# Optimization experiments

Hardware: AMD Instinct MI355X
Metric: run time of the kernel (lower is better)

The kernel has to match this reference:

```python
import jax, jax.numpy as jnp
import numpy as np

H = 16
D_MODEL = 1024
D_K = D_MODEL // H
B, S = 4, 2048


def setup_inputs() -> dict:
    key = jax.random.key(0)
    ks = jax.random.split(key, 8)
    scale = 1.0 / np.sqrt(D_MODEL)
    return {
        "query": jax.random.normal(ks[0], (B, S, D_MODEL), dtype=jnp.float32),
        "key": jax.random.normal(ks[1], (B, S, D_MODEL), dtype=jnp.float32),
        "value": jax.random.normal(ks[2], (B, S, D_MODEL), dtype=jnp.float32),
        "A": jnp.zeros((1,), dtype=jnp.float32),
        "Wq": jax.random.normal(ks[3], (D_MODEL, D_MODEL), dtype=jnp.float32) * scale,
        "bq": jnp.zeros((D_MODEL,), dtype=jnp.float32),
        "Wk": jax.random.normal(ks[4], (D_MODEL, D_MODEL), dtype=jnp.float32) * scale,
        "bk": jnp.zeros((D_MODEL,), dtype=jnp.float32),
        "Wv": jax.random.normal(ks[5], (D_MODEL, D_MODEL), dtype=jnp.float32) * scale,
        "bv": jnp.zeros((D_MODEL,), dtype=jnp.float32),
        "Wo": jax.random.normal(ks[6], (D_MODEL, D_MODEL), dtype=jnp.float32) * scale,
        "bo": jnp.zeros((D_MODEL,), dtype=jnp.float32),
    }


def reference(query, key, value, A, Wq, bq, Wk, bk, Wv, bv, Wo, bo):
    nb = query.shape[0]

    def proj(x, W, b):
        # torch Linear: x @ W.T + b, then view(B, S, H, D_K) and transpose -> [B, H, S, D_K]
        y = jnp.einsum('bsd,ed->bse', x, W) + b
        return y.reshape(nb, -1, H, D_K).transpose(0, 2, 1, 3)

    q = proj(query, Wq, bq)
    k = proj(key, Wk, bk)
    v = proj(value, Wv, bv)

    # NOTE: original code has NO 1/sqrt(d_k) scaling, no mask, no dropout.
    scores = jnp.einsum('bhqd,bhkd->bhqk', q, k)  # [B,H,S,S]
    p_attn = jax.nn.softmax(scores, axis=-1)
    x = jnp.einsum('bhqk,bhkd->bhqd', p_attn, v)  # [B,H,S,D_K]

    x = x.transpose(0, 2, 1, 3).reshape(nb, -1, H * D_K)  # [B,S,d_model]
    out = jnp.einsum('bsd,ed->bse', x, Wo) + bo
    loss = jnp.asarray(0.0, dtype=out.dtype)
    return (out, loss)
```

## Files before the change

kernel.cpp:

```cpp
#include <hip/hip_runtime.h>

typedef unsigned short u16;
typedef _Float16 half8 __attribute__((ext_vector_type(8)));
typedef _Float16 h2 __attribute__((ext_vector_type(2)));
typedef float f32x4 __attribute__((ext_vector_type(4)));
typedef u16 u16x4 __attribute__((ext_vector_type(4)));
typedef u16 u16x8 __attribute__((ext_vector_type(8)));

#define MFMAH(a, b, c) __builtin_amdgcn_mfma_f32_16x16x32_f16(a, b, c, 0, 0, 0)

constexpr float LOG2E = 1.44269504088896f;
constexpr float THR = 12.0f;

__device__ __forceinline__ u16 f2h(float f) {
  _Float16 h = (_Float16)f;
  return __builtin_bit_cast(u16, h);
}
__device__ __forceinline__ h2 pkrtz(float a, float b) {
  return __builtin_bit_cast(h2, __builtin_amdgcn_cvt_pkrtz(a, b));
}

__device__ __forceinline__ void gload_lds16(const void* g, void* l) {
  __builtin_amdgcn_global_load_lds(
      (const __attribute__((address_space(1))) void*)g,
      (__attribute__((address_space(3))) void*)l,
      16, 0, 0);
}

__global__ __launch_bounds__(256) void conv_f32_f16(const float* __restrict__ in,
                                                    u16* __restrict__ out, int n8) {
  int i = blockIdx.x * 256 + threadIdx.x;
  const int stride = gridDim.x * 256;
  for (; i < n8; i += stride) {
    const float4 a = reinterpret_cast<const float4*>(in)[2 * i];
    const float4 b = reinterpret_cast<const float4*>(in)[2 * i + 1];
    u16x8 o;
    o[0] = f2h(a.x); o[1] = f2h(a.y); o[2] = f2h(a.z); o[3] = f2h(a.w);
    o[4] = f2h(b.x); o[5] = f2h(b.y); o[6] = f2h(b.z); o[7] = f2h(b.w);
    reinterpret_cast<u16x8*>(out)[i] = o;
  }
}

template <int MODE>
__global__ __launch_bounds__(256) void gemm_bt(const u16* __restrict__ A,
                                               const u16* __restrict__ Bw,
                                               const float* __restrict__ bias,
                                               void* __restrict__ Cv,
                                               int M, int N, int K, float scale) {
  __shared__ u16 As[128 * 32];
  __shared__ u16 Bs[128 * 32];
  const int tid = threadIdx.x;
  const int lane = tid & 63;
  const int l16 = lane & 15, lhi = lane >> 4;
  const int wid = tid >> 6;
  const int wm = wid >> 1, wn = wid & 1;
  const int bm0 = blockIdx.y * 128;
  const int bn0 = blockIdx.x * 128;

  const int c0 = tid, c1 = tid + 256;
  const u16* Ag0 = A + (size_t)(bm0 + (c0 >> 2)) * K + (c0 & 3) * 8;
  const u16* Ag1 = A + (size_t)(bm0 + (c1 >> 2)) * K + (c1 & 3) * 8;
  const u16* Bg0 = Bw + (size_t)(bn0 + (c0 >> 2)) * K + (c0 & 3) * 8;
  const u16* Bg1 = Bw + (size_t)(bn0 + (c1 >> 2)) * K + (c1 & 3) * 8;

  f32x4 acc[4][4] = {};

  for (int kt = 0; kt < K; kt += 32) {
    gload_lds16(Ag0 + kt, &As[c0 * 8]);
    gload_lds16(Ag1 + kt, &As[c1 * 8]);
    gload_lds16(Bg0 + kt, &Bs[c0 * 8]);
    gload_lds16(Bg1 + kt, &Bs[c1 * 8]);
    __syncthreads();
    half8 af[4], bf[4];
#pragma unroll
    for (int f = 0; f < 4; ++f)
      af[f] = *reinterpret_cast<const half8*>(&As[(wm * 64 + f * 16 + l16) * 32 + lhi * 8]);
#pragma unroll
    for (int f = 0; f < 4; ++f)
      bf[f] = *reinterpret_cast<const half8*>(&Bs[(wn * 64 + f * 16 + l16) * 32 + lhi * 8]);
#pragma unroll
    for (int i = 0; i < 4; ++i)
#pragma unroll
      for (int j = 0; j < 4; ++j)
        acc[i][j] = MFMAH(af[i], bf[j], acc[i][j]);
    __syncthreads();
  }

#pragma unroll
  for (int i = 0; i < 4; ++i) {
    const int m0 = bm0 + wm * 64 + i * 16 + lhi * 4;
#pragma unroll
    for (int j = 0; j < 4; ++j) {
      const int n = bn0 + wn * 64 + j * 16 + l16;
      const float bb = bias[n];
      if (MODE == 0) {
        float* Cf = (float*)Cv;
#pragma unroll
        for (int r = 0; r < 4; ++r)
          Cf[(size_t)(m0 + r) * N + n] = acc[i][j][r] + bb;
      } else if (MODE == 2) {
        u16* C = (u16*)Cv;
        u16x4 pack;
#pragma unroll
        for (int r = 0; r < 4; ++r) pack[r] = f2h(acc[i][j][r] + bb);
        const int head = (m0 >> 11) * 16 + (n >> 6);
        const int s0 = m0 & 2047;
        const int d = n & 63;
        const size_t idx = (((size_t)head * 64 + (s0 >> 5)) * 64 + d) * 32 +
                           ((s0 >> 2) & 3) * 8 + ((s0 >> 4) & 1) * 4;
        *reinterpret_cast<u16x4*>(&C[idx]) = pack;
      } else {
        u16* C = (u16*)Cv;
#pragma unroll
        for (int r = 0; r < 4; ++r) {
          const int m = m0 + r;
          const size_t idx =
              ((size_t)((m >> 11) * 16 + (n >> 6)) * 2048 + (m & 2047)) * 64 + (n & 63);
          C[idx] = f2h((acc[i][j][r] + bb) * scale);
        }
      }
    }
  }
}

__global__ __launch_bounds__(256, 4) void attn_fwd(const u16* __restrict__ Q,
                                                   const u16* __restrict__ Kh,
                                                   const u16* __restrict__ VL,
                                                   u16* __restrict__ X) {
  __shared__ u16 Ks[2][4096];
  __shared__ u16 Vs[2][4096];

  const int tid = threadIdx.x, lane = tid & 63, w = tid >> 6;
  const int l16 = lane & 15, lhi = lane >> 4;
  const int blk = blockIdx.x;
  const int xcd = blk & 7, wi = blk >> 3;
  const int bh = (xcd << 3) | (wi >> 4);
  const int qt = wi & 15;
  const int b = bh >> 4, h = bh & 15;

  const size_t qrow0 = (size_t)bh * 2048 + qt * 128 + w * 32;
  half8 qf[2][2];
#pragma unroll
  for (int fq = 0; fq < 2; ++fq)
#pragma unroll
    for (int ks = 0; ks < 2; ++ks)
      qf[fq][ks] = *reinterpret_cast<const half8*>(
          &Q[(qrow0 + fq * 16 + l16) * 64 + ks * 32 + lhi * 8]);

  f32x4 o[2][4] = {};
  float mrow[2] = {-1e30f, -1e30f};
  float ssum[2] = {0.0f, 0.0f};

  const u16* Kb = Kh + (size_t)bh * 2048 * 64;
  const u16* VLh = VL + (size_t)bh * 64 * 64 * 32;

#define STAGE_KV(bufidx, tt)                                                      \
  do {                                                                            \
    const int kb0_ = (tt) * 64;                                                   \
    _Pragma("unroll")                                                             \
    for (int ii_ = 0; ii_ < 2; ++ii_) {                                           \
      const int c_ = tid + ii_ * 256;                                             \
      const int r_ = c_ >> 3, cb_ = c_ & 7;                                       \
      gload_lds16(Kb + (size_t)(kb0_ + r_) * 64 + ((cb_ ^ (r_ & 7)) << 3),        \
                  &Ks[bufidx][c_ * 8]);                                           \
      gload_lds16(VLh + (size_t)(tt) * 4096 + c_ * 8, &Vs[bufidx][c_ * 8]);       \
    }                                                                             \
  } while (0)

  STAGE_KV(0, 0);
  __syncthreads();

  for (int t = 0; t < 32; ++t) {
    const int cur = t & 1;
    if (t < 31) STAGE_KV(cur ^ 1, t + 1);
    f32x4 sc[2][4] = {};
#pragma unroll
    for (int fk = 0; fk < 4; ++fk) {
      const int row = fk * 16 + l16;
#pragma unroll
      for (int ks = 0; ks < 2; ++ks) {
        const int off = (row * 64 + ks * 32 + lhi * 8) ^ ((row & 7) << 3);
        const half8 kf = *reinterpret_cast<const half8*>(&Ks[cur][off]);
#pragma unroll
        for (int fq = 0; fq < 2; ++fq) sc[fq][fk] = MFMAH(kf, qf[fq][ks], sc[fq][fk]);
      }
    }
    float lm[2];
#pragma unroll
    for (int fq = 0; fq < 2; ++fq) {
      float v = sc[fq][0][0];
#pragma unroll
      for (int fk = 0; fk < 4; ++fk)
#pragma unroll
        for (int r = 0; r < 4; ++r) v = fmaxf(v, sc[fq][fk][r]);
      lm[fq] = v;
    }
    const int trig = (lm[0] > mrow[0] + THR) || (lm[1] > mrow[1] + THR);
    if (__any(trig)) {
#pragma unroll
      for (int fq = 0; fq < 2; ++fq) {
        float rm = lm[fq];
        rm = fmaxf(rm, __shfl_xor(rm, 16));
        rm = fmaxf(rm, __shfl_xor(rm, 32));
        const float nm = fmaxf(mrow[fq], rm);
        const float scl = __builtin_amdgcn_exp2f(mrow[fq] - nm);
        mrow[fq] = nm;
        ssum[fq] *= scl;
        float sb[4];
#pragma unroll
        for (int r = 0; r < 4; ++r) sb[r] = __shfl(scl, lhi * 4 + r);
#pragma unroll
        for (int fd = 0; fd < 4; ++fd)
#pragma unroll
          for (int r = 0; r < 4; ++r) o[fq][fd][r] *= sb[r];
      }
    }
    half8 pa2[2][2];
#pragma unroll
    for (int fq = 0; fq < 2; ++fq) {
      union { half8 v[2]; h2 hh[8]; } uu;
#pragma unroll
      for (int fk = 0; fk < 4; ++fk) {
        const float p0 = __builtin_amdgcn_exp2f(sc[fq][fk][0] - mrow[fq]);
        const float p1 = __builtin_amdgcn_exp2f(sc[fq][fk][1] - mrow[fq]);
        const float p2 = __builtin_amdgcn_exp2f(sc[fq][fk][2] - mrow[fq]);
        const float p3 = __builtin_amdgcn_exp2f(sc[fq][fk][3] - mrow[fq]);
        ssum[fq] += (p0 + p1) + (p2 + p3);
        uu.hh[fk * 2 + 0] = pkrtz(p0, p1);
        uu.hh[fk * 2 + 1] = pkrtz(p2, p3);
      }
      pa2[fq][0] = uu.v[0];
      pa2[fq][1] = uu.v[1];
    }
#pragma unroll
    for (int fd = 0; fd < 4; ++fd)
#pragma unroll
      for (int ts = 0; ts < 2; ++ts) {
        const half8 vf = *reinterpret_cast<const half8*>(
            &Vs[cur][ts * 2048 + (fd * 16 + l16) * 32 + lhi * 8]);
#pragma unroll
        for (int fq = 0; fq < 2; ++fq) o[fq][fd] = MFMAH(pa2[fq][ts], vf, o[fq][fd]);
      }
    __syncthreads();
  }
#undef STAGE_KV

#pragma unroll
  for (int fq = 0; fq < 2; ++fq) {
    float ss = ssum[fq];
    ss += __shfl_xor(ss, 16);
    ss += __shfl_xor(ss, 32);
    float iv[4];
#pragma unroll
    for (int r = 0; r < 4; ++r) iv[r] = 1.0f / __shfl(ss, lhi * 4 + r);
#pragma unroll
    for (int r = 0; r < 4; ++r) {
      const int q = qt * 128 + w * 32 + fq * 16 + lhi * 4 + r;
#pragma unroll
      for (int fd = 0; fd < 4; ++fd) {
        const int col = h * 64 + fd * 16 + l16;
        X[((size_t)b * 2048 + q) * 1024 + col] = f2h(o[fq][fd][r] * iv[r]);
      }
    }
  }
}

__global__ void write_loss(float* out, int idx) { out[idx] = 0.0f; }

extern "C" void kernel_launch(void* const* d_in, const int* in_sizes, int n_in,
                              void* d_out, int out_size, void* d_ws, size_t ws_size,
                              hipStream_t stream) {
  const float* q_f  = (const float*)d_in[0];
  const float* k_f  = (const float*)d_in[1];
  const float* v_f  = (const float*)d_in[2];
  const float* Wq_f = (const float*)d_in[4];
  const float* bq   = (const float*)d_in[5];
  const float* Wk_f = (const float*)d_in[6];
  const float* bk   = (const float*)d_in[7];
  const float* Wv_f = (const float*)d_in[8];
  const float* bv   = (const float*)d_in[9];
  const float* Wo_f = (const float*)d_in[10];
  const float* bo   = (const float*)d_in[11];

  const int SZ = 4 * 2048 * 1024;
  const int SW = 1024 * 1024;

  u16* ws = (u16*)d_ws;
  u16* qb   = ws;
  u16* kbuf = qb + SZ;
  u16* vbuf = kbuf + SZ;
  u16* wqb = vbuf + SZ;
  u16* wkb = wqb + SW;
  u16* wvb = wkb + SW;
  u16* wob = wvb + SW;
  u16* Qb  = wob + SW;
  u16* Kb  = Qb + SZ;
  u16* VLb = Kb + SZ;
  u16* Xb  = VLb + SZ;
  const size_t need_bytes = (size_t)(7 * SZ + 4 * SW) * 2;
  if (ws_size < need_bytes) return;

  conv_f32_f16<<<2048, 256, 0, stream>>>(q_f, qb, SZ / 8);
  conv_f32_f16<<<2048, 256, 0, stream>>>(k_f, kbuf, SZ / 8);
  conv_f32_f16<<<2048, 256, 0, stream>>>(v_f, vbuf, SZ / 8);
  conv_f32_f16<<<512, 256, 0, stream>>>(Wq_f, wqb, SW / 8);
  conv_f32_f16<<<512, 256, 0, stream>>>(Wk_f, wkb, SW / 8);
  conv_f32_f16<<<512, 256, 0, stream>>>(Wv_f, wvb, SW / 8);
  conv_f32_f16<<<512, 256, 0, stream>>>(Wo_f, wob, SW / 8);

  dim3 gg(1024 / 128, 8192 / 128);
  gemm_bt<1><<<gg, 256, 0, stream>>>(qb, wqb, bq, Qb, 8192, 1024, 1024, LOG2E);
  gemm_bt<1><<<gg, 256, 0, stream>>>(kbuf, wkb, bk, Kb, 8192, 1024, 1024, 1.0f);
  gemm_bt<2><<<gg, 256, 0, stream>>>(vbuf, wvb, bv, VLb, 8192, 1024, 1024, 1.0f);

  attn_fwd<<<dim3(1024), 256, 0, stream>>>(Qb, Kb, VLb, Xb);

  gemm_bt<0><<<gg, 256, 0, stream>>>(Xb, wob, bo, d_out, 8192, 1024, 1024, 1.0f);
  write_loss<<<1, 1, 0, stream>>>((float*)d_out, out_size - 1);
}
```

Baseline: 252.4 us.

## Merge conversion kernels, swizzle V layout for LDS reads, tree-reduce row max

The seven separate fp32-to-fp16 conversion launches become two: one for the Q/K/V activations and one for the four weight matrices. This cuts launch overhead and tail effects. The V projection epilogue now writes an XOR-swizzled layout, and the attention kernel reads V from shared memory with a matching swizzle to avoid LDS bank conflicts. The per-tile row max is rewritten as a shallower tree of fmax operations to shorten the dependency chain.

After: 252.8 us. About the same (+0.2%).

```diff
diff --git a/kernel.cpp b/kernel.cpp
--- a/kernel.cpp
+++ b/kernel.cpp
@@ -27,17 +27,46 @@
       16, 0, 0);
 }
 
-__global__ __launch_bounds__(256) void conv_f32_f16(const float* __restrict__ in,
-                                                    u16* __restrict__ out, int n8) {
+__device__ __forceinline__ void conv_block(const float* __restrict__ in,
+                                           u16* __restrict__ out, int i) {
+  const float4 a = reinterpret_cast<const float4*>(in)[2 * i];
+  const float4 b = reinterpret_cast<const float4*>(in)[2 * i + 1];
+  u16x8 o;
+  o[0] = f2h(a.x); o[1] = f2h(a.y); o[2] = f2h(a.z); o[3] = f2h(a.w);
+  o[4] = f2h(b.x); o[5] = f2h(b.y); o[6] = f2h(b.z); o[7] = f2h(b.w);
+  reinterpret_cast<u16x8*>(out)[i] = o;
+}
+
+__global__ __launch_bounds__(256) void conv_qkv(const float* __restrict__ q,
+                                                const float* __restrict__ k,
+                                                const float* __restrict__ v,
+                                                u16* __restrict__ qo, u16* __restrict__ ko,
+                                                u16* __restrict__ vo, int n8) {
   int i = blockIdx.x * 256 + threadIdx.x;
   const int stride = gridDim.x * 256;
-  for (; i < n8; i += stride) {
-    const float4 a = reinterpret_cast<const float4*>(in)[2 * i];
-    const float4 b = reinterpret_cast<const float4*>(in)[2 * i + 1];
-    u16x8 o;
-    o[0] = f2h(a.x); o[1] = f2h(a.y); o[2] = f2h(a.z); o[3] = f2h(a.w);
-    o[4] = f2h(b.x); o[5] = f2h(b.y); o[6] = f2h(b.z); o[7] = f2h(b.w);
-    reinterpret_cast<u16x8*>(out)[i] = o;
+  for (; i < 3 * n8; i += stride) {
+    const int sel = i / n8, j = i - sel * n8;
+    if (sel == 0) conv_block(q, qo, j);
+    else if (sel == 1) conv_block(k, ko, j);
+    else conv_block(v, vo, j);
+  }
+}
+
+__global__ __launch_bounds__(256) void conv_w4(const float* __restrict__ w0,
+                                               const float* __restrict__ w1,
+                                               const float* __restrict__ w2,
+                                               const float* __restrict__ w3,
+                                               u16* __restrict__ o0, u16* __restrict__ o1,
+                                               u16* __restrict__ o2, u16* __restrict__ o3,
+                                               int n8) {
+  int i = blockIdx.x * 256 + threadIdx.x;
+  const int stride = gridDim.x * 256;
+  for (; i < 4 * n8; i += stride) {
+    const int sel = i / n8, j = i - sel * n8;
+    if (sel == 0) conv_block(w0, o0, j);
+    else if (sel == 1) conv_block(w1, o1, j);
+    else if (sel == 2) conv_block(w2, o2, j);
+    else conv_block(w3, o3, j);
   }
 }
 
@@ -106,8 +135,10 @@
         const int head = (m0 >> 11) * 16 + (n >> 6);
         const int s0 = m0 & 2047;
         const int d = n & 63;
-        const size_t idx = (((size_t)head * 64 + (s0 >> 5)) * 64 + d) * 32 +
-                           ((s0 >> 2) & 3) * 8 + ((s0 >> 4) & 1) * 4;
+        const int within =
+            ((s0 >> 5) & 1) * 2048 + d * 32 + ((s0 >> 2) & 3) * 8 + ((s0 >> 4) & 1) * 4;
+        const int sw = within ^ ((d & 7) << 3);
+        const size_t idx = (size_t)head * 131072 + (size_t)(s0 >> 6) * 4096 + sw;
         *reinterpret_cast<u16x4*>(&C[idx]) = pack;
       } else {
         u16* C = (u16*)Cv;
@@ -188,12 +219,14 @@
     float lm[2];
 #pragma unroll
     for (int fq = 0; fq < 2; ++fq) {
-      float v = sc[fq][0][0];
-#pragma unroll
-      for (int fk = 0; fk < 4; ++fk)
-#pragma unroll
-        for (int r = 0; r < 4; ++r) v = fmaxf(v, sc[fq][fk][r]);
-      lm[fq] = v;
+      float a0 = fmaxf(fmaxf(sc[fq][0][0], sc[fq][0][1]), sc[fq][0][2]);
+      float a1 = fmaxf(fmaxf(sc[fq][0][3], sc[fq][1][0]), sc[fq][1][1]);
+      float a2 = fmaxf(fmaxf(sc[fq][1][2], sc[fq][1][3]), sc[fq][2][0]);
+      float a3 = fmaxf(fmaxf(sc[fq][2][1], sc[fq][2][2]), sc[fq][2][3]);
+      float a4 = fmaxf(fmaxf(sc[fq][3][0], sc[fq][3][1]), sc[fq][3][2]);
+      float b0 = fmaxf(fmaxf(a0, a1), a2);
+      float b1 = fmaxf(fmaxf(a3, a4), sc[fq][3][3]);
+      lm[fq] = fmaxf(b0, b1);
     }
     const int trig = (lm[0] > mrow[0] + THR) || (lm[1] > mrow[1] + THR);
     if (__any(trig)) {
@@ -236,8 +269,8 @@
     for (int fd = 0; fd < 4; ++fd)
 #pragma unroll
       for (int ts = 0; ts < 2; ++ts) {
-        const half8 vf = *reinterpret_cast<const half8*>(
-            &Vs[cur][ts * 2048 + (fd * 16 + l16) * 32 + lhi * 8]);
+        const int va = (ts * 2048 + (fd * 16 + l16) * 32 + lhi * 8) ^ ((l16 & 7) << 3);
+        const half8 vf = *reinterpret_cast<const half8*>(&Vs[cur][va]);
 #pragma unroll
         for (int fq = 0; fq < 2; ++fq) o[fq][fd] = MFMAH(pa2[fq][ts], vf, o[fq][fd]);
       }
@@ -300,13 +333,8 @@
   const size_t need_bytes = (size_t)(7 * SZ + 4 * SW) * 2;
   if (ws_size < need_bytes) return;
 
-  conv_f32_f16<<<2048, 256, 0, stream>>>(q_f, qb, SZ / 8);
-  conv_f32_f16<<<2048, 256, 0, stream>>>(k_f, kbuf, SZ / 8);
-  conv_f32_f16<<<2048, 256, 0, stream>>>(v_f, vbuf, SZ / 8);
-  conv_f32_f16<<<512, 256, 0, stream>>>(Wq_f, wqb, SW / 8);
-  conv_f32_f16<<<512, 256, 0, stream>>>(Wk_f, wkb, SW / 8);
-  conv_f32_f16<<<512, 256, 0, stream>>>(Wv_f, wvb, SW / 8);
-  conv_f32_f16<<<512, 256, 0, stream>>>(Wo_f, wob, SW / 8);
+  conv_qkv<<<2048, 256, 0, stream>>>(q_f, k_f, v_f, qb, kbuf, vbuf, SZ / 8);
+  conv_w4<<<1024, 256, 0, stream>>>(Wq_f, Wk_f, Wv_f, Wo_f, wqb, wkb, wvb, wob, SW / 8);
 
   dim3 gg(1024 / 128, 8192 / 128);
   gemm_bt<1><<<gg, 256, 0, stream>>>(qb, wqb, bq, Qb, 8192, 1024, 1024, LOG2E);
```
